# Optimization experiments

Hardware: AMD Instinct MI355X
Metric: run time of the kernel (lower is better)

The kernel has to match this reference:

```python
import jax, jax.numpy as jnp
import numpy as np

B = 1024
M = 131072          # memory_size
K = 256             # key_dim
CHOOSE_K = 256
BETA = 1e-08
EPS = 0.001


def setup_inputs() -> dict:
    key = jax.random.key(0)
    k1, k2, k3 = jax.random.split(key, 3)
    q = jax.random.normal(k1, (B, K), dtype=jnp.float32)
    mk = jax.random.normal(k2, (M, K), dtype=jnp.float32)
    memory_key = mk / jnp.linalg.norm(mk, axis=1, keepdims=True)  # unit-norm keys as in update_memory
    # __init__: first half values = 1 (real), second half = 0 (fake)
    memory_values = jnp.concatenate([jnp.ones((M // 2,), jnp.float32),
                                     jnp.zeros((M - M // 2,), jnp.float32)])
    # hist starts near 1e-5; add small positive noise so p_c is non-degenerate
    memory_hist = 1e-05 + 1e-05 * jax.random.uniform(k3, (M,), dtype=jnp.float32)
    return {"q": q, "memory_key": memory_key,
            "memory_values": memory_values, "memory_hist": memory_hist}


def reference(q, memory_key, memory_values, memory_hist):
    # similarities: [B, M]
    similarities = jnp.matmul(q, memory_key.T)
    p_x_given_c_unnorm = jnp.exp(similarities)
    hist_b = memory_hist + BETA
    p_c = hist_b / jnp.sum(hist_b)                       # [M]
    p_c_given_x = p_x_given_c_unnorm * p_c               # [B, M]
    p_c_given_x_approx, idxs = jax.lax.top_k(p_c_given_x, CHOOSE_K)  # [B, k]
    vals = memory_values[idxs]                           # gather, [B, k]
    p_y_given_x_unnorm = jnp.sum(vals * p_c_given_x_approx, axis=1)
    p_y_given_x = p_y_given_x_unnorm / jnp.sum(p_c_given_x_approx, axis=1)
    return jnp.clip(p_y_given_x, EPS, 1.0 - EPS)
```

## Files before the change

### kernel.cpp

```cpp
#include <hip/hip_runtime.h>
#include <math.h>
#include <stdint.h>

#define MMEM 131072
#define KDIM 256
#define NB   1024
#define TOPK 256
#define BETA_F 1e-08f
#define NTILE 2048
#define OVFCAP 65536
#define SLOTS 4
#define SBINS 1024
#define SCAP  2560
#define SBCAP 256

typedef _Float16 f16x8 __attribute__((ext_vector_type(8)));
typedef float    f32x4 __attribute__((ext_vector_type(4)));

__device__ __forceinline__ void gload16(const void* g, void* l) {
  __builtin_amdgcn_global_load_lds(
      (const __attribute__((address_space(1))) uint32_t*)g,
      (__attribute__((address_space(3))) uint32_t*)l, 16, 0, 0);
}

#define NQ16 (NB * KDIM / 16)
#define NM16 (MMEM * KDIM / 16)
#define CVTB ((NQ16 + NM16) / 256)
__global__ __launch_bounds__(256) void prep_kernel(const float* __restrict__ q,
                                                   const float* __restrict__ mk,
                                                   _Float16* __restrict__ qh,
                                                   _Float16* __restrict__ mkh,
                                                   const float* __restrict__ hist,
                                                   float* __restrict__ partials,
                                                   float* __restrict__ partials_log) {
  const int b = blockIdx.x;
  if (b < CVTB) {
    int i = b * 256 + threadIdx.x;
    const float* in; _Float16* out; size_t j;
    if (i < NQ16) { in = q;  out = qh;  j = (size_t)i; }
    else          { in = mk; out = mkh; j = (size_t)(i - NQ16); }
    const float4* src = (const float4*)(in + j * 16);
    union { _Float16 h[16]; uint4 u[2]; } p;
    #pragma unroll
    for (int k = 0; k < 4; ++k) {
      float4 v = src[k];
      p.h[k * 4 + 0] = (_Float16)v.x; p.h[k * 4 + 1] = (_Float16)v.y;
      p.h[k * 4 + 2] = (_Float16)v.z; p.h[k * 4 + 3] = (_Float16)v.w;
    }
    uint4* dst = (uint4*)(out + j * 16);
    dst[0] = p.u[0];
    dst[1] = p.u[1];
    return;
  }
  const int bid = b - CVTB;
  float s = 0.f, sl = 0.f;
  for (int i = bid * 256 + threadIdx.x; i < MMEM; i += 256 * 256) {
    float h = hist[i] + BETA_F;
    s += h;
    sl += logf(h);
  }
  #pragma unroll
  for (int off = 32; off > 0; off >>= 1) {
    s  += __shfl_down(s, off);
    sl += __shfl_down(sl, off);
  }
  __shared__ float ws[4], wsl[4];
  int lane = threadIdx.x & 63, wid = threadIdx.x >> 6;
  if (lane == 0) { ws[wid] = s; wsl[wid] = sl; }
  __syncthreads();
  if (threadIdx.x == 0) {
    partials[bid]     = ws[0] + ws[1] + ws[2] + ws[3];
    partials_log[bid] = wsl[0] + wsl[1] + wsl[2] + wsl[3];
  }
}

__global__ __launch_bounds__(256) void logpc_final_kernel(const float* __restrict__ hist,
                                                          const float* __restrict__ partials,
                                                          const float* __restrict__ partials_log,
                                                          float* __restrict__ logpc,
                                                          float* __restrict__ out_sum,
                                                          float* __restrict__ out_thresh,
                                                          uint32_t* __restrict__ ovf_cnt,
                                                          float z0) {
  __shared__ float ws[4], wsl[4];
  const int tid = threadIdx.x;
  float s = partials[tid];
  float sl = (blockIdx.x == 0) ? partials_log[tid] : 0.f;
  #pragma unroll
  for (int off = 32; off > 0; off >>= 1) {
    s  += __shfl_down(s, off);
    sl += __shfl_down(sl, off);
  }
  int lane = tid & 63, wid = tid >> 6;
  if (lane == 0) { ws[wid] = s; wsl[wid] = sl; }
  __syncthreads();
  const float sum = ws[0] + ws[1] + ws[2] + ws[3];
  const int i = blockIdx.x * 256 + tid;
  logpc[i] = logf(hist[i] + BETA_F) - logf(sum);
  if (blockIdx.x == 0 && tid == 0) {
    float suml = wsl[0] + wsl[1] + wsl[2] + wsl[3];
    *out_sum = sum;
    *out_thresh = suml / (float)MMEM - logf(sum) + z0;
    *ovf_cnt = 0u;
  }
}

__global__ __launch_bounds__(256, 3) void gemm_kernel(const _Float16* __restrict__ qh,
                                                      const _Float16* __restrict__ mkh,
                                                      const float* __restrict__ logpc,
                                                      const float* __restrict__ values,
                                                      const float* __restrict__ thresh,
                                                      float2* __restrict__ cand,
                                                      uint8_t* __restrict__ cnt,
                                                      int4* __restrict__ ovf,
                                                      uint32_t* __restrict__ ovf_cnt) {
  __shared__ _Float16 As[3][4096];
  __shared__ _Float16 Bs[3][4096];

  const int t    = threadIdx.x;
  const int lane = t & 63;
  const int wave = t >> 6;
  const int wr   = (wave & 1) * 64;
  const int wc   = (wave >> 1) * 64;
  const int lm   = lane & 15;
  const int lk   = lane >> 4;

  const int wg  = blockIdx.x;
  const int lg  = ((wg & 7) << 10) | (wg >> 3);
  const int row0 = (lg & 7) << 7;
  const int col0 = (lg >> 3) << 7;

  const int r0q = t >> 2;
  const int cc  = (t & 3) ^ ((r0q >> 1) & 3);

  const char* gA0 = (const char*)qh  + ((size_t)(row0 + r0q)      * KDIM) * 2 + cc * 16;
  const char* gA1 = (const char*)qh  + ((size_t)(row0 + 64 + r0q) * KDIM) * 2 + cc * 16;
  const char* gB0 = (const char*)mkh + ((size_t)(col0 + r0q)      * KDIM) * 2 + cc * 16;
  const char* gB1 = (const char*)mkh + ((size_t)(col0 + 64 + r0q) * KDIM) * 2 + cc * 16;

  int offA[4], offB[4];
  #pragma unroll
  for (int i = 0; i < 4; ++i) {
    int ar = wr + i * 16 + lm;
    offA[i] = ar * 64 + ((lk ^ ((ar >> 1) & 3)) * 16);
    int br = wc + i * 16 + lm;
    offB[i] = br * 64 + ((lk ^ ((br >> 1) & 3)) * 16);
  }

  const float tv = *thresh;
  float lpv[4], vv[4];
  #pragma unroll
  for (int j = 0; j < 4; ++j) {
    lpv[j] = logpc[col0 + wc + j * 16 + lm];
    vv[j]  = values[col0 + wc + j * 16 + lm];
  }
  asm volatile("s_waitcnt vmcnt(0)" ::: "memory");

  f32x4 acc[4][4];
  #pragma unroll
  for (int i = 0; i < 4; i++)
    #pragma unroll
    for (int j = 0; j < 4; j++)
      acc[i][j] = (f32x4){0.f, 0.f, 0.f, 0.f};

  auto stage = [&](int buf, int chunk) {
    const size_t ko = (size_t)chunk * 64;
    gload16(gA0 + ko, (char*)&As[buf][0] + t * 16);
    gload16(gA1 + ko, (char*)&As[buf][0] + 4096 + t * 16);
    gload16(gB0 + ko, (char*)&Bs[buf][0] + t * 16);
    gload16(gB1 + ko, (char*)&Bs[buf][0] + 4096 + t * 16);
  };

  stage(0, 0);
  stage(1, 1);
  asm volatile("s_waitcnt vmcnt(4)" ::: "memory");
  __builtin_amdgcn_s_barrier();
  asm volatile("" ::: "memory");

  #pragma unroll
  for (int it = 0; it < 8; ++it) {
    const int cur = it % 3;
    const char* Ab = (const char*)&As[cur][0];
    const char* Bb = (const char*)&Bs[cur][0];
    f16x8 af[4], bf[4];
    #pragma unroll
    for (int i = 0; i < 4; ++i) af[i] = *(const f16x8*)(Ab + offA[i]);
    #pragma unroll
    for (int j = 0; j < 4; ++j) bf[j] = *(const f16x8*)(Bb + offB[j]);
    if (it + 2 < 8) stage((it + 2) % 3, it + 2);
    __builtin_amdgcn_s_setprio(1);
    #pragma unroll
    for (int i = 0; i < 4; ++i)
      #pragma unroll
      for (int j = 0; j < 4; ++j)
        acc[i][j] = __builtin_amdgcn_mfma_f32_16x16x32_f16(af[i], bf[j], acc[i][j], 0, 0, 0);
    __builtin_amdgcn_s_setprio(0);
    if (it < 7) {
      if (it + 2 < 8) asm volatile("s_waitcnt vmcnt(4)" ::: "memory");
      else            asm volatile("s_waitcnt vmcnt(0)" ::: "memory");
      __builtin_amdgcn_s_barrier();
      asm volatile("" ::: "memory");
    }
  }

  const int coltile = (col0 + wc) >> 6;
  const uint32_t ltm = (1u << lm) - 1u;
  const int shift = lane & 48;
  #pragma unroll
  for (int i = 0; i < 4; ++i) {
    #pragma unroll
    for (int r4 = 0; r4 < 4; ++r4) {
      const int row = row0 + wr + i * 16 + lk * 4 + r4;
      float sv[4];
      #pragma unroll
      for (int j = 0; j < 4; ++j) sv[j] = acc[i][j][r4] + lpv[j];
      float mx = fmaxf(fmaxf(sv[0], sv[1]), fmaxf(sv[2], sv[3]));
      uint32_t anym = (uint32_t)((__ballot(mx >= tv) >> shift) & 0xFFFFull);
      const size_t bucket = (size_t)row * NTILE + coltile;
      if (anym == 0u) {
        if (lm == 0) cnt[bucket] = 0;
        continue;
      }
      uint32_t gm[4];
      int tot = 0;
      #pragma unroll
      for (int j = 0; j < 4; ++j) {
        gm[j] = (uint32_t)((__ballot(sv[j] >= tv) >> shift) & 0xFFFFull);
        tot += __popc(gm[j]);
      }
      if (lm == 0) cnt[bucket] = (uint8_t)(tot < SLOTS ? tot : SLOTS);
      float2* bs = cand + bucket * SLOTS;
      int prev = 0;
      #pragma unroll
      for (int j = 0; j < 4; ++j) {
        if ((gm[j] >> lm) & 1u) {
          int k = prev + __popc(gm[j] & ltm);
          if (k < SLOTS) {
            bs[k] = make_float2(sv[j], vv[j]);
          } else {
            int col = col0 + wc + j * 16 + lm;
            uint32_t p = atomicAdd(ovf_cnt, 1u);
            if (p < OVFCAP) ovf[p] = make_int4(row, col, __float_as_int(sv[j]),
                                               __float_as_int(vv[j]));
          }
        }
        prev += __popc(gm[j]);
      }
    }
  }
}

__global__ __launch_bounds__(512) void select_kernel(const float2* __restrict__ cand,
                                                     const uint8_t* __restrict__ cnt,
                                                     const int4* __restrict__ ovf,
                                                     const uint32_t* __restrict__ ovf_cnt,
                                                     const float* __restrict__ thresh,
                                                     float* __restrict__ out) {
  __shared__ uint32_t hist[SBINS];
  __shared__ float cs_s[SCAP];
  __shared__ float cs_v[SCAP];
  __shared__ uint32_t csum[32];
  __shared__ int s_bstar, s_above, s_ccnt, s_bcnt;
  __shared__ float bin_s[SBCAP];
  __shared__ float bin_v[SBCAP];
  __shared__ float red_p[8], red_vp[8];

  const int tid = threadIdx.x;
  const int row = blockIdx.x;
  const float tv = *thresh;
  const int novf = (int)min(*ovf_cnt, (uint32_t)OVFCAP);

  for (int i = tid; i < SBINS; i += 512) hist[i] = 0;
  if (tid == 0) { s_ccnt = 0; s_bcnt = 0; }
  __syncthreads();

  {
    const uint32_t* cnt32 = (const uint32_t*)(cnt + (size_t)row * NTILE);
    for (int w = tid; w < NTILE / 4; w += 512) {
      uint32_t cw = cnt32[w];
      if (cw == 0u) continue;
      #pragma unroll
      for (int s4 = 0; s4 < 4; ++s4) {
        int c = (int)((cw >> (8 * s4)) & 0xFFu);
        if (c > 0) {
          size_t bucket = (size_t)row * NTILE + (w * 4 + s4);
          const float4* b4 = (const float4*)(cand + bucket * SLOTS);
          float4 lo = b4[0];
          float4 hi = b4[1];
          #pragma unroll
          for (int k = 0; k < 4; k++) {
            if (k < c) {
              float s = (k == 0) ? lo.x : (k == 1) ? lo.z : (k == 2) ? hi.x : hi.z;
              float v = (k == 0) ? lo.y : (k == 1) ? lo.w : (k == 2) ? hi.y : hi.w;
              int b = (int)((s - tv) * 256.0f);
              b = b < 0 ? 0 : (b > SBINS - 1 ? SBINS - 1 : b);
              atomicAdd(&hist[b], 1u);
              int pos = atomicAdd(&s_ccnt, 1);
              if (pos < SCAP) { cs_s[pos] = s; cs_v[pos] = v; }
            }
          }
        }
      }
    }
  }
  for (int i = tid; i < novf; i += 512) {
    int4 e = ovf[i];
    if (e.x == row) {
      float s = __int_as_float(e.z);
      float v = __int_as_float(e.w);
      int b = (int)((s - tv) * 256.0f);
      b = b < 0 ? 0 : (b > SBINS - 1 ? SBINS - 1 : b);
      atomicAdd(&hist[b], 1u);
      int pos = atomicAdd(&s_ccnt, 1);
      if (pos < SCAP) { cs_s[pos] = s; cs_v[pos] = v; }
    }
  }
  __syncthreads();

  if (tid < 32) {
    uint32_t s = 0;
    for (int b = 0; b < 32; b++) s += hist[tid * 32 + b];
    csum[tid] = s;
  }
  __syncthreads();
  if (tid == 0) {
    uint32_t cum = 0;
    int bstar = 0; uint32_t above = 0;
    for (int c = 31; c >= 0; c--) {
      if (cum + csum[c] >= TOPK) {
        for (int b = 31; b >= 0; b--) {
          uint32_t h = hist[c * 32 + b];
          if (cum + h >= TOPK) { bstar = c * 32 + b; above = cum; goto found; }
          cum += h;
        }
      }
      cum += csum[c];
    }
    bstar = 0; above = cum - hist[0];
  found:
    s_bstar = bstar;
    s_above = (int)above;
  }
  __syncthreads();
  const int bstar = s_bstar;
  int rneed = TOPK - s_above;
  const int ctot = s_ccnt;

  float psum = 0.f, vpsum = 0.f;
  if (ctot <= SCAP) {
    for (int i = tid; i < ctot; i += 512) {
      float s = cs_s[i];
      float v = cs_v[i];
      int b = (int)((s - tv) * 256.0f);
      b = b < 0 ? 0 : (b > SBINS - 1 ? SBINS - 1 : b);
      if (b > bstar) {
        float p = __expf(s);
        psum += p;
        vpsum += p * v;
      } else if (b == bstar) {
        int pos = atomicAdd(&s_bcnt, 1);
        if (pos < SBCAP) { bin_s[pos] = s; bin_v[pos] = v; }
      }
    }
  } else {
    for (int tile = tid; tile < NTILE; tile += 512) {
      size_t bucket = (size_t)row * NTILE + tile;
      int c = (int)cnt[bucket];
      const float2* bs = cand + bucket * SLOTS;
      for (int k = 0; k < c; k++) {
        float2 e = bs[k];
        int b = (int)((e.x - tv) * 256.0f);
        b = b < 0 ? 0 : (b > SBINS - 1 ? SBINS - 1 : b);
        if (b > bstar) {
          float p = __expf(e.x);
          psum += p;
          vpsum += p * e.y;
        } else if (b == bstar) {
          int pos = atomicAdd(&s_bcnt, 1);
          if (pos < SBCAP) { bin_s[pos] = e.x; bin_v[pos] = e.y; }
        }
      }
    }
    for (int i = tid; i < novf; i += 512) {
      int4 e = ovf[i];
      if (e.x == row) {
        float s = __int_as_float(e.z);
        float v = __int_as_float(e.w);
        int b = (int)((s - tv) * 256.0f);
        b = b < 0 ? 0 : (b > SBINS - 1 ? SBINS - 1 : b);
        if (b > bstar) {
          float p = __expf(s);
          psum += p;
          vpsum += p * v;
        } else if (b == bstar) {
          int pos = atomicAdd(&s_bcnt, 1);
          if (pos < SBCAP) { bin_s[pos] = s; bin_v[pos] = v; }
        }
      }
    }
  }
  __syncthreads();

  int c2 = s_bcnt < SBCAP ? s_bcnt : SBCAP;
  int n2 = 1;
  while (n2 < c2) n2 <<= 1;
  for (int i = c2 + tid; i < n2; i += 512) { bin_s[i] = -INFINITY; bin_v[i] = 0.f; }
  __syncthreads();

  for (int size = 2; size <= n2; size <<= 1) {
    for (int stride = size >> 1; stride > 0; stride >>= 1) {
      for (int i = tid; i < n2; i += 512) {
        int j = i ^ stride;
        if (j > i) {
          float si = bin_s[i], sj = bin_s[j];
          float vi = bin_v[i], vj = bin_v[j];
          bool igt = (si > sj) || (si == sj && vi > vj);
          bool desc = ((i & size) == 0);
          if (desc ? !igt : igt) {
            bin_s[i] = sj; bin_s[j] = si;
            bin_v[i] = vj; bin_v[j] = vi;
          }
        }
      }
      __syncthreads();
    }
  }

  int take = rneed < c2 ? rneed : c2;
  if (take < 0) take = 0;
  for (int i = tid; i < take; i += 512) {
    float p = __expf(bin_s[i]);
    psum += p;
    vpsum += p * bin_v[i];
  }

  #pragma unroll
  for (int off = 32; off > 0; off >>= 1) {
    psum  += __shfl_down(psum, off);
    vpsum += __shfl_down(vpsum, off);
  }
  int lane = tid & 63, wid = tid >> 6;
  if (lane == 0) { red_p[wid] = psum; red_vp[wid] = vpsum; }
  __syncthreads();
  if (tid == 0) {
    float P = 0.f, V = 0.f;
    for (int w = 0; w < 8; w++) { P += red_p[w]; V += red_vp[w]; }
    float r = V / P;
    r = fminf(fmaxf(r, 1e-3f), 1.0f - 1e-3f);
    out[row] = r;
  }
}

extern "C" void kernel_launch(void* const* d_in, const int* in_sizes, int n_in,
                              void* d_out, int out_size, void* d_ws, size_t ws_size,
                              hipStream_t stream) {
  const float* q      = (const float*)d_in[0];
  const float* mk     = (const float*)d_in[1];
  const float* values = (const float*)d_in[2];
  const float* hist   = (const float*)d_in[3];
  float* out = (float*)d_out;

  float*    ws_sum   = (float*)d_ws;
  float*    ws_thr   = (float*)((char*)d_ws + 64);
  uint32_t* ovf_cnt  = (uint32_t*)((char*)d_ws + 128);
  float*    partials = (float*)((char*)d_ws + 4096);
  float*    partialsl= (float*)((char*)d_ws + 8192);
  float*    logpc    = (float*)((char*)d_ws + 16384);
  _Float16* qh       = (_Float16*)((char*)d_ws + 540672);
  _Float16* mkh      = (_Float16*)((char*)d_ws + 1064960);
  uint8_t*  cnt      = (uint8_t*)((char*)d_ws + 68173824ull);
  int4*     ovf      = (int4*)((char*)d_ws + 76562432ull);
  float2*   cand     = (float2*)((char*)d_ws + 77611008ull);

  const float z0 = 2.4176f;

  prep_kernel<<<CVTB + 256, 256, 0, stream>>>(q, mk, qh, mkh, hist, partials, partialsl);
  logpc_final_kernel<<<MMEM / 256, 256, 0, stream>>>(hist, partials, partialsl, logpc,
                                                     ws_sum, ws_thr, ovf_cnt, z0);
  gemm_kernel<<<8192, 256, 0, stream>>>(qh, mkh, logpc, values, ws_thr,
                                        cand, cnt, ovf, ovf_cnt);
  select_kernel<<<NB, 512, 0, stream>>>(cand, cnt, ovf, ovf_cnt, ws_thr, out);
}
```

Before: 355.6 us.

## Fold logpc/threshold kernel into GEMM prologue and drop per-row early-exit ballot

Result: no change. 350.2 us (-1.5%).

```diff
diff --git a/kernel.cpp b/kernel.cpp
--- a/kernel.cpp
+++ b/kernel.cpp
@@ -32,7 +32,8 @@
                                                    _Float16* __restrict__ mkh,
                                                    const float* __restrict__ hist,
                                                    float* __restrict__ partials,
-                                                   float* __restrict__ partials_log) {
+                                                   float* __restrict__ partials_log,
+                                                   uint32_t* __restrict__ ovf_cnt) {
   const int b = blockIdx.x;
   if (b < CVTB) {
     int i = b * 256 + threadIdx.x;
@@ -71,51 +72,25 @@
   if (threadIdx.x == 0) {
     partials[bid]     = ws[0] + ws[1] + ws[2] + ws[3];
     partials_log[bid] = wsl[0] + wsl[1] + wsl[2] + wsl[3];
-  }
-}
-
-__global__ __launch_bounds__(256) void logpc_final_kernel(const float* __restrict__ hist,
-                                                          const float* __restrict__ partials,
-                                                          const float* __restrict__ partials_log,
-                                                          float* __restrict__ logpc,
-                                                          float* __restrict__ out_sum,
-                                                          float* __restrict__ out_thresh,
-                                                          uint32_t* __restrict__ ovf_cnt,
-                                                          float z0) {
-  __shared__ float ws[4], wsl[4];
-  const int tid = threadIdx.x;
-  float s = partials[tid];
-  float sl = (blockIdx.x == 0) ? partials_log[tid] : 0.f;
-  #pragma unroll
-  for (int off = 32; off > 0; off >>= 1) {
-    s  += __shfl_down(s, off);
-    sl += __shfl_down(sl, off);
-  }
-  int lane = tid & 63, wid = tid >> 6;
-  if (lane == 0) { ws[wid] = s; wsl[wid] = sl; }
-  __syncthreads();
-  const float sum = ws[0] + ws[1] + ws[2] + ws[3];
-  const int i = blockIdx.x * 256 + tid;
-  logpc[i] = logf(hist[i] + BETA_F) - logf(sum);
-  if (blockIdx.x == 0 && tid == 0) {
-    float suml = wsl[0] + wsl[1] + wsl[2] + wsl[3];
-    *out_sum = sum;
-    *out_thresh = suml / (float)MMEM - logf(sum) + z0;
-    *ovf_cnt = 0u;
+    if (bid == 0) *ovf_cnt = 0u;
   }
 }
 
 __global__ __launch_bounds__(256, 3) void gemm_kernel(const _Float16* __restrict__ qh,
                                                       const _Float16* __restrict__ mkh,
-                                                      const float* __restrict__ logpc,
+                                                      const float* __restrict__ hist,
                                                       const float* __restrict__ values,
-                                                      const float* __restrict__ thresh,
+                                                      const float* __restrict__ partials,
+                                                      const float* __restrict__ partials_log,
+                                                      float* __restrict__ ws_thr,
                                                       float2* __restrict__ cand,
                                                       uint8_t* __restrict__ cnt,
                                                       int4* __restrict__ ovf,
-                                                      uint32_t* __restrict__ ovf_cnt) {
+                                                      uint32_t* __restrict__ ovf_cnt,
+                                                      float z0) {
   __shared__ _Float16 As[3][4096];
   __shared__ _Float16 Bs[3][4096];
+  __shared__ float ws4[4], wsl4[4];
 
   const int t    = threadIdx.x;
   const int lane = t & 63;
@@ -147,12 +122,28 @@
     offB[i] = br * 64 + ((lk ^ ((br >> 1) & 3)) * 16);
   }
 
-  const float tv = *thresh;
+  {
+    float ps  = partials[t];
+    float psl = partials_log[t];
+    #pragma unroll
+    for (int off = 32; off > 0; off >>= 1) {
+      ps  += __shfl_down(ps, off);
+      psl += __shfl_down(psl, off);
+    }
+    if ((lane & 63) == 0) { ws4[wave] = ps; wsl4[wave] = psl; }
+  }
+  __syncthreads();
+  const float sum    = ws4[0] + ws4[1] + ws4[2] + ws4[3];
+  const float logSum = logf(sum);
+  const float tv = (wsl4[0] + wsl4[1] + wsl4[2] + wsl4[3]) / (float)MMEM - logSum + z0;
+  if (t == 0) *ws_thr = tv;
+
   float lpv[4], vv[4];
   #pragma unroll
   for (int j = 0; j < 4; ++j) {
-    lpv[j] = logpc[col0 + wc + j * 16 + lm];
-    vv[j]  = values[col0 + wc + j * 16 + lm];
+    int col = col0 + wc + j * 16 + lm;
+    lpv[j] = logf(hist[col] + BETA_F) - logSum;
+    vv[j]  = values[col];
   }
   asm volatile("s_waitcnt vmcnt(0)" ::: "memory");
 
@@ -212,22 +203,15 @@
     for (int r4 = 0; r4 < 4; ++r4) {
       const int row = row0 + wr + i * 16 + lk * 4 + r4;
       float sv[4];
-      #pragma unroll
-      for (int j = 0; j < 4; ++j) sv[j] = acc[i][j][r4] + lpv[j];
-      float mx = fmaxf(fmaxf(sv[0], sv[1]), fmaxf(sv[2], sv[3]));
-      uint32_t anym = (uint32_t)((__ballot(mx >= tv) >> shift) & 0xFFFFull);
-      const size_t bucket = (size_t)row * NTILE + coltile;
-      if (anym == 0u) {
-        if (lm == 0) cnt[bucket] = 0;
-        continue;
-      }
       uint32_t gm[4];
       int tot = 0;
       #pragma unroll
       for (int j = 0; j < 4; ++j) {
+        sv[j] = acc[i][j][r4] + lpv[j];
         gm[j] = (uint32_t)((__ballot(sv[j] >= tv) >> shift) & 0xFFFFull);
         tot += __popc(gm[j]);
       }
+      const size_t bucket = (size_t)row * NTILE + coltile;
       if (lm == 0) cnt[bucket] = (uint8_t)(tot < SLOTS ? tot : SLOTS);
       float2* bs = cand + bucket * SLOTS;
       int prev = 0;
@@ -460,12 +444,10 @@
   const float* hist   = (const float*)d_in[3];
   float* out = (float*)d_out;
 
-  float*    ws_sum   = (float*)d_ws;
   float*    ws_thr   = (float*)((char*)d_ws + 64);
   uint32_t* ovf_cnt  = (uint32_t*)((char*)d_ws + 128);
   float*    partials = (float*)((char*)d_ws + 4096);
   float*    partialsl= (float*)((char*)d_ws + 8192);
-  float*    logpc    = (float*)((char*)d_ws + 16384);
   _Float16* qh       = (_Float16*)((char*)d_ws + 540672);
   _Float16* mkh      = (_Float16*)((char*)d_ws + 1064960);
   uint8_t*  cnt      = (uint8_t*)((char*)d_ws + 68173824ull);
@@ -474,10 +456,9 @@
 
   const float z0 = 2.4176f;
 
-  prep_kernel<<<CVTB + 256, 256, 0, stream>>>(q, mk, qh, mkh, hist, partials, partialsl);
-  logpc_final_kernel<<<MMEM / 256, 256, 0, stream>>>(hist, partials, partialsl, logpc,
-                                                     ws_sum, ws_thr, ovf_cnt, z0);
-  gemm_kernel<<<8192, 256, 0, stream>>>(qh, mkh, logpc, values, ws_thr,
-                                        cand, cnt, ovf, ovf_cnt);
+  prep_kernel<<<CVTB + 256, 256, 0, stream>>>(q, mk, qh, mkh, hist,
+                                              partials, partialsl, ovf_cnt);
+  gemm_kernel<<<8192, 256, 0, stream>>>(qh, mkh, hist, values, partials, partialsl,
+                                        ws_thr, cand, cnt, ovf, ovf_cnt, z0);
   select_kernel<<<NB, 512, 0, stream>>>(cand, cnt, ovf, ovf_cnt, ws_thr, out);
 }
```
